# Kernel optimization log

Hardware: AMD Instinct MI355X
Metric: run time of the kernel (lower is better)

Reference implementation:

```python
import jax, jax.numpy as jnp
import numpy as np


def _rotate_half(x):
    x1, x2 = jnp.split(x, 2, axis=-1)
    return jnp.concatenate([-x2, x1], axis=-1)


def _rope_tables(seq_len, head_dim, base=10000.0):
    inv_freq = 1.0 / (base ** (jnp.arange(0, head_dim, 2, dtype=jnp.float32) / head_dim))
    t = jnp.arange(seq_len, dtype=jnp.float32)
    freqs = jnp.outer(t, inv_freq)  # [S, head_dim/2]
    # torch .repeat(...,2) tiles along last dim -> concat
    cos = jnp.concatenate([jnp.cos(freqs), jnp.cos(freqs)], axis=-1)  # [S, head_dim]
    sin = jnp.concatenate([jnp.sin(freqs), jnp.sin(freqs)], axis=-1)
    return cos[None, None], sin[None, None]  # [1,1,S,head_dim]


def setup_inputs() -> dict:
    key = jax.random.key(0)
    ks = jax.random.split(key, 5)
    B, S, D = 2, 2048, 2048
    sd = 1.0 / np.sqrt(D)
    return {
        "x": jax.random.normal(ks[0], (B, S, D), dtype=jnp.float32),
        "Wq": jax.random.normal(ks[1], (D, D), dtype=jnp.float32) * sd,
        "Wk": jax.random.normal(ks[2], (D, D), dtype=jnp.float32) * sd,
        "Wv": jax.random.normal(ks[3], (D, D), dtype=jnp.float32) * sd,
        "Wo": jax.random.normal(ks[4], (D, D), dtype=jnp.float32) * sd,
        "n_heads": 16,
    }


def reference(x, Wq, Wk, Wv, Wo, n_heads):
    B, S, D = x.shape
    hd = D // n_heads
    # projections (torch Linear: x @ W.T)
    def proj(W):
        return (x @ W.T).reshape(B, S, n_heads, hd).transpose(0, 2, 1, 3)  # [B,H,S,hd]
    q, k, v = proj(Wq), proj(Wk), proj(Wv)
    cos, sin = _rope_tables(S, hd)
    q = q * cos + _rotate_half(q) * sin
    k = k * cos + _rotate_half(k) * sin
    scale = 1.0 / np.sqrt(hd)
    scores = jnp.einsum('bhsd,bhtd->bhst', q, k) * scale  # [B,H,S,S]
    causal = jnp.triu(jnp.ones((S, S), dtype=bool), k=1)
    scores = jnp.where(causal[None, None], -jnp.inf, scores)
    attn = jax.nn.softmax(scores, axis=-1)
    out = jnp.einsum('bhst,bhtd->bhsd', attn, v)
    out = out.transpose(0, 2, 1, 3).reshape(B, S, D)
    return out @ Wo.T
```

## Files before the change

kernel.cpp:

```cpp
#include <hip/hip_runtime.h>
#include <hip/hip_bf16.h>
#include <math.h>

typedef __attribute__((ext_vector_type(8))) short bf16x8;
typedef __attribute__((ext_vector_type(4))) float f32x4;

#define GLB_CAST(p) ((const __attribute__((address_space(1))) void*)(p))
#define LDS_CAST(p) ((__attribute__((address_space(3))) void*)(p))

__global__ void cvt_f32_bf16(const float* __restrict__ s, __hip_bfloat16* __restrict__ d, int n) {
    int i = (blockIdx.x * 256 + threadIdx.x) * 8;
    if (i >= n) return;
    float4 a = *(const float4*)(s + i);
    float4 b = *(const float4*)(s + i + 4);
    float t[8] = {a.x, a.y, a.z, a.w, b.x, b.y, b.z, b.w};
    union { unsigned short u[8]; uint4 v; } o;
#pragma unroll
    for (int j = 0; j < 8; ++j) {
        __hip_bfloat16 h = __float2bfloat16(t[j]);
        o.u[j] = *(unsigned short*)&h;
    }
    *(uint4*)(d + i) = o.v;
}

template <int EPI>
__global__ __launch_bounds__(256, 2)
void gemm_bt(const __hip_bfloat16* __restrict__ A,
             const __hip_bfloat16* __restrict__ Bt,
             void* __restrict__ Cout)
{
    const int K = 2048;
    __shared__ __hip_bfloat16 As[128 * 32];
    __shared__ __hip_bfloat16 Bs[128 * 32];
    const int tid = threadIdx.x;
    const int w = tid >> 6, l = tid & 63;
    const int m0 = blockIdx.x * 128, n0 = blockIdx.y * 128;
    const int wr = w >> 1, wc = w & 1;
    const int lr = l & 15, kh = l >> 4;

    f32x4 acc[4][4] = {};

    for (int kt = 0; kt < 64; ++kt) {
        const int kb = kt * 32;
#pragma unroll
        for (int i = 0; i < 2; ++i) {
            const int s = i * 256 + tid;
            const int r = s >> 2, ks = (s & 3) * 8;
            __builtin_amdgcn_global_load_lds(GLB_CAST(A + (size_t)(m0 + r) * K + kb + ks),
                                             LDS_CAST(As + (size_t)(i * 256 + w * 64) * 8),
                                             16, 0, 0);
            __builtin_amdgcn_global_load_lds(GLB_CAST(Bt + (size_t)(n0 + r) * K + kb + ks),
                                             LDS_CAST(Bs + (size_t)(i * 256 + w * 64) * 8),
                                             16, 0, 0);
        }
        __syncthreads();
        bf16x8 af[4], bfr[4];
#pragma unroll
        for (int m = 0; m < 4; ++m)
            af[m] = *(const bf16x8*)(As + (wr * 64 + m * 16 + lr) * 32 + kh * 8);
#pragma unroll
        for (int n = 0; n < 4; ++n)
            bfr[n] = *(const bf16x8*)(Bs + (wc * 64 + n * 16 + lr) * 32 + kh * 8);
#pragma unroll
        for (int m = 0; m < 4; ++m)
#pragma unroll
            for (int n = 0; n < 4; ++n)
                acc[m][n] = __builtin_amdgcn_mfma_f32_16x16x32_bf16(af[m], bfr[n], acc[m][n], 0, 0, 0);
        __syncthreads();
    }

#pragma unroll
    for (int m = 0; m < 4; ++m) {
        const int r0 = m0 + wr * 64 + m * 16 + kh * 4;
#pragma unroll
        for (int n = 0; n < 4; ++n) {
            const int c = n0 + wc * 64 + n * 16 + lr;
#pragma unroll
            for (int j = 0; j < 4; ++j) {
                const int r = r0 + j;
                const float v = acc[m][n][j];
                if (EPI == 0) {
                    const int b = r >> 11, sy = r & 2047, h = c >> 7, dd = c & 127;
                    ((__hip_bfloat16*)Cout)[((size_t)(b * 16 + h) * 2048 + sy) * 128 + dd] =
                        __float2bfloat16(v);
                } else if (EPI == 2) {
                    const int b = r >> 11, sy = r & 2047, h = c >> 7, dd = c & 127;
                    ((__hip_bfloat16*)Cout)[((size_t)(b * 16 + h) * 128 + dd) * 2048 + sy] =
                        __float2bfloat16(v);
                } else {
                    ((float*)Cout)[(size_t)r * 2048 + c] = v;
                }
            }
        }
    }
}

__global__ void rope_qk(__hip_bfloat16* __restrict__ Q, __hip_bfloat16* __restrict__ Kk) {
    const int row = blockIdx.x * 4 + (threadIdx.x >> 6);
    const int j = threadIdx.x & 63;
    const int s = row & 2047;
    const float inv = expf((float)j * (-0.14391156831212787f));
    float sn, c;
    sincosf((float)s * inv, &sn, &c);
    const size_t base = (size_t)row * 128;
    float q1 = __bfloat162float(Q[base + j]);
    float q2 = __bfloat162float(Q[base + 64 + j]);
    Q[base + j]      = __float2bfloat16(q1 * c - q2 * sn);
    Q[base + 64 + j] = __float2bfloat16(q2 * c + q1 * sn);
    float k1 = __bfloat162float(Kk[base + j]);
    float k2 = __bfloat162float(Kk[base + 64 + j]);
    Kk[base + j]      = __float2bfloat16(k1 * c - k2 * sn);
    Kk[base + 64 + j] = __float2bfloat16(k2 * c + k1 * sn);
}

__global__ __launch_bounds__(256, 4)
void flash_part(const __hip_bfloat16* __restrict__ Q,
                const __hip_bfloat16* __restrict__ K,
                const __hip_bfloat16* __restrict__ Vt,
                __hip_bfloat16* __restrict__ AO,
                __hip_bfloat16* __restrict__ OP,
                float* __restrict__ ML)
{
    const int bh = blockIdx.x;
    const int u  = blockIdx.y;
    const int tid = threadIdx.x, w = tid >> 6, l = tid & 63;
    const int lr = l & 15, hi = l >> 4;

    int G, part, P;
    if (u < 32)      { G = 24 + (u >> 2);            part = u & 3;       P = 4; }
    else if (u < 56) { int v = u - 32; G = 16 + v/3; part = v % 3;       P = 3; }
    else if (u < 72) { int v = u - 56; G = 8 + (v>>1); part = v & 1;     P = 2; }
    else             { G = u - 72;                   part = 0;           P = 1; }
    const int nt = 2 * G + 2;
    const int t0 = (part * nt) / P, t1 = ((part + 1) * nt) / P;
    const bool split = (P > 1);
    const int qb = G * 64 + w * 16;

    const __hip_bfloat16* Qb = Q  + (size_t)bh * 2048 * 128;
    const __hip_bfloat16* Kb = K  + (size_t)bh * 2048 * 128;
    const __hip_bfloat16* Vb = Vt + (size_t)bh * 128 * 2048;

    __shared__ __align__(16) __hip_bfloat16 Ks[2][32 * 128];
    __shared__ __align__(16) __hip_bfloat16 Vs[2][128 * 32];
    __shared__ __align__(16) __hip_bfloat16 Pl[4][16 * 40];
    __hip_bfloat16* Pw = &Pl[w][0];

    bf16x8 qf[4];
#pragma unroll
    for (int kk = 0; kk < 4; ++kk)
        qf[kk] = *(const bf16x8*)(Qb + (size_t)(qb + lr) * 128 + kk * 32 + hi * 8);

    int rK[2], cK[2], rV[2], cV[2];
#pragma unroll
    for (int i = 0; i < 2; ++i) {
        const int ci = i * 4 + w;
        rK[i] = ci * 4 + (l >> 4);
        cK[i] = ((l & 15) ^ (rK[i] & 7)) * 8;
        rV[i] = ci * 16 + (l >> 2);
        cV[i] = ((l & 3) ^ (rV[i] & 3)) * 8;
    }
    const int rsw7 = lr & 7, vsw3 = lr & 3;

#define STAGE(buf, t)                                                                        \
    {                                                                                        \
        const int kv0_ = (t) * 32;                                                           \
        _Pragma("unroll")                                                                    \
        for (int i = 0; i < 2; ++i) {                                                        \
            __builtin_amdgcn_global_load_lds(                                                \
                GLB_CAST(Kb + (size_t)(kv0_ + rK[i]) * 128 + cK[i]),                         \
                LDS_CAST(&Ks[buf][(i * 4 + w) * 512]), 16, 0, 0);                            \
            __builtin_amdgcn_global_load_lds(                                                \
                GLB_CAST(Vb + (size_t)rV[i] * 2048 + kv0_ + cV[i]),                          \
                LDS_CAST(&Vs[buf][(i * 4 + w) * 512]), 16, 0, 0);                            \
        }                                                                                    \
    }

    f32x4 o[8] = {};
    float mrow[4] = {-1e30f, -1e30f, -1e30f, -1e30f};
    float lrow[4] = {0.f, 0.f, 0.f, 0.f};
    const float scale = 0.08838834764831845f;

    int cur = 0;
    STAGE(0, t0);
    __syncthreads();

    for (int t = t0; t < t1; ++t) {
        if (t + 1 < t1) STAGE(cur ^ 1, t + 1);
        const __hip_bfloat16* Kc = &Ks[cur][0];
        const __hip_bfloat16* Vc = &Vs[cur][0];
        const int kv0 = t * 32;

        f32x4 sf[2] = {};
#pragma unroll
        for (int f = 0; f < 2; ++f)
#pragma unroll
            for (int kk = 0; kk < 4; ++kk) {
                const bf16x8 kf = *(const bf16x8*)(Kc + (f * 16 + lr) * 128 +
                                                   ((kk * 4 + hi) ^ rsw7) * 8);
                sf[f] = __builtin_amdgcn_mfma_f32_16x16x32_bf16(qf[kk], kf, sf[f], 0, 0, 0);
            }

        float alpha[4];
#pragma unroll
        for (int j = 0; j < 4; ++j) {
            const int q = qb + hi * 4 + j;
            float s0v = sf[0][j] * scale; if (kv0 + lr > q)      s0v = -1e30f;
            float s1v = sf[1][j] * scale; if (kv0 + 16 + lr > q) s1v = -1e30f;
            float mx = fmaxf(s0v, s1v);
#pragma unroll
            for (int dd = 1; dd < 16; dd <<= 1)
                mx = fmaxf(mx, __shfl_xor(mx, dd));
            const float mnew = fmaxf(mrow[j], mx);
            alpha[j] = __expf(mrow[j] - mnew);
            mrow[j] = mnew;
            const float p0 = __expf(s0v - mnew);
            const float p1 = __expf(s1v - mnew);
            float rs = p0 + p1;
#pragma unroll
            for (int dd = 1; dd < 16; dd <<= 1)
                rs += __shfl_xor(rs, dd);
            lrow[j] = lrow[j] * alpha[j] + rs;
            Pw[(hi * 4 + j) * 40 + lr]      = __float2bfloat16(p0);
            Pw[(hi * 4 + j) * 40 + 16 + lr] = __float2bfloat16(p1);
        }
#pragma unroll
        for (int dn = 0; dn < 8; ++dn)
#pragma unroll
            for (int j = 0; j < 4; ++j) o[dn][j] *= alpha[j];

        const bf16x8 pf = *(const bf16x8*)(Pw + lr * 40 + hi * 8);
#pragma unroll
        for (int dn = 0; dn < 8; ++dn) {
            const bf16x8 vf = *(const bf16x8*)(Vc + (dn * 16 + lr) * 32 + (hi ^ vsw3) * 8);
            o[dn] = __builtin_amdgcn_mfma_f32_16x16x32_bf16(pf, vf, o[dn], 0, 0, 0);
        }
        __syncthreads();
        cur ^= 1;
    }
#undef STAGE

    if (!split) {
#pragma unroll
        for (int j = 0; j < 4; ++j) {
            const float inv = 1.0f / lrow[j];
            const int q = qb + hi * 4 + j;
            const size_t rb = ((size_t)(bh >> 4) * 2048 + q) * 2048 + (size_t)(bh & 15) * 128;
#pragma unroll
            for (int dn = 0; dn < 8; ++dn)
                AO[rb + dn * 16 + lr] = __float2bfloat16(o[dn][j] * inv);
        }
    } else {
        const int base = (G < 16) ? (G - 8) * 2 : ((G < 24) ? 16 + (G - 16) * 3
                                                            : 40 + (G - 24) * 4);
        const int pidx = bh * 72 + base + part;
#pragma unroll
        for (int j = 0; j < 4; ++j) {
            const int row = w * 16 + hi * 4 + j;
#pragma unroll
            for (int dn = 0; dn < 8; ++dn)
                OP[((size_t)pidx * 64 + row) * 128 + dn * 16 + lr] = __float2bfloat16(o[dn][j]);
            if (lr == 0) {
                ML[((size_t)pidx * 64 + row) * 2]     = mrow[j];
                ML[((size_t)pidx * 64 + row) * 2 + 1] = lrow[j];
            }
        }
    }
}

__global__ void flash_merge(const __hip_bfloat16* __restrict__ OP,
                            const float* __restrict__ ML,
                            __hip_bfloat16* __restrict__ AO)
{
    const int gi = blockIdx.x % 24, bh = blockIdx.x / 24;
    const int G = 8 + gi;
    const int P = (G < 16) ? 2 : ((G < 24) ? 3 : 4);
    const int base = (G < 16) ? (G - 8) * 2 : ((G < 24) ? 16 + (G - 16) * 3
                                                        : 40 + (G - 24) * 4);
    const int pidx0 = bh * 72 + base;
    const int t = threadIdx.x, r = t >> 2, c0 = (t & 3) * 32;

    float m[4], lv[4];
    float M = -1e30f;
#pragma unroll
    for (int p = 0; p < 4; ++p) if (p < P) {
        m[p]  = ML[((size_t)(pidx0 + p) * 64 + r) * 2];
        lv[p] = ML[((size_t)(pidx0 + p) * 64 + r) * 2 + 1];
        M = fmaxf(M, m[p]);
    }
    float wgt[4];
    float den = 0.f;
#pragma unroll
    for (int p = 0; p < 4; ++p) if (p < P) {
        wgt[p] = __expf(m[p] - M);
        den += lv[p] * wgt[p];
    }
    const float inv = 1.0f / den;

    const int q = G * 64 + r;
    __hip_bfloat16* out = AO + ((size_t)(bh >> 4) * 2048 + q) * 2048 + (size_t)(bh & 15) * 128 + c0;

#pragma unroll
    for (int ch = 0; ch < 4; ++ch) {
        float acc[8] = {0.f, 0.f, 0.f, 0.f, 0.f, 0.f, 0.f, 0.f};
#pragma unroll
        for (int p = 0; p < 4; ++p) if (p < P) {
            const bf16x8 v = *(const bf16x8*)(OP + ((size_t)(pidx0 + p) * 64 + r) * 128 + c0 + ch * 8);
#pragma unroll
            for (int i = 0; i < 8; ++i) {
                __hip_bfloat16 hv;
                *(short*)&hv = v[i];
                acc[i] += __bfloat162float(hv) * wgt[p];
            }
        }
        union { unsigned short us[8]; bf16x8 v; } rr;
#pragma unroll
        for (int i = 0; i < 8; ++i) {
            __hip_bfloat16 hv = __float2bfloat16(acc[i] * inv);
            rr.us[i] = *(unsigned short*)&hv;
        }
        *(bf16x8*)(out + ch * 8) = rr.v;
    }
}

extern "C" void kernel_launch(void* const* d_in, const int* in_sizes, int n_in,
                              void* d_out, int out_size, void* d_ws, size_t ws_size,
                              hipStream_t stream) {
    (void)in_sizes; (void)n_in; (void)out_size; (void)ws_size;
    const float* x  = (const float*)d_in[0];
    const float* Wq = (const float*)d_in[1];
    const float* Wk = (const float*)d_in[2];
    const float* Wv = (const float*)d_in[3];
    const float* Wo = (const float*)d_in[4];

    char* p = (char*)d_ws;
    auto carve = [&](size_t bytes) -> char* {
        char* r = p;
        p += (bytes + 255) & ~(size_t)255;
        return r;
    };
    __hip_bfloat16* xb  = (__hip_bfloat16*)carve(4096ull * 2048 * 2);
    __hip_bfloat16* Wqb = (__hip_bfloat16*)carve(2048ull * 2048 * 2);
    __hip_bfloat16* Wkb = (__hip_bfloat16*)carve(2048ull * 2048 * 2);
    __hip_bfloat16* Wvb = (__hip_bfloat16*)carve(2048ull * 2048 * 2);
    __hip_bfloat16* Wob = (__hip_bfloat16*)carve(2048ull * 2048 * 2);
    __hip_bfloat16* Qb  = (__hip_bfloat16*)carve(32ull * 2048 * 128 * 2);
    __hip_bfloat16* Kb  = (__hip_bfloat16*)carve(32ull * 2048 * 128 * 2);
    __hip_bfloat16* Vtb = (__hip_bfloat16*)carve(32ull * 128 * 2048 * 2);
    __hip_bfloat16* OPb = (__hip_bfloat16*)carve(32ull * 72 * 64 * 128 * 2);
    float*          MLb = (float*)carve(32ull * 72 * 64 * 2 * 4);

    cvt_f32_bf16<<<4096, 256, 0, stream>>>(x,  xb,  4096 * 2048);
    cvt_f32_bf16<<<2048, 256, 0, stream>>>(Wq, Wqb, 2048 * 2048);
    cvt_f32_bf16<<<2048, 256, 0, stream>>>(Wk, Wkb, 2048 * 2048);
    cvt_f32_bf16<<<2048, 256, 0, stream>>>(Wv, Wvb, 2048 * 2048);
    cvt_f32_bf16<<<2048, 256, 0, stream>>>(Wo, Wob, 2048 * 2048);

    dim3 gg(32, 16);
    gemm_bt<0><<<gg, 256, 0, stream>>>(xb, Wqb, Qb);
    gemm_bt<0><<<gg, 256, 0, stream>>>(xb, Wkb, Kb);
    gemm_bt<2><<<gg, 256, 0, stream>>>(xb, Wvb, Vtb);

    rope_qk<<<16384, 256, 0, stream>>>(Qb, Kb);

    flash_part<<<dim3(32, 80), 256, 0, stream>>>(Qb, Kb, Vtb, xb , OPb, MLb);
    flash_merge<<<768, 256, 0, stream>>>(OPb, MLb, xb );

    gemm_bt<1><<<gg, 256, 0, stream>>>(xb, Wob, (float*)d_out);
}
```

Baseline: 356.2 us.

## Compute transposed S tiles in flash attention and pass P through register shuffles

The QK^T MFMA operands are swapped so each lane owns one query row's scores across the KV block. This turns the per-row max and sum reductions into two cross-lane shuffles and lets the P fragment be built by register shuffles instead of an LDS round-trip. It also adds a lazy rescale that skips the O rescaling while the running max has grown by no more than 8, and switches the RoPE kernel to fast __expf/__sincosf intrinsics. The cost is extra shuffles to rebuild the P fragment and broadcast alpha, and some lost precision in the RoPE angles.

```diff
diff --git a/kernel.cpp b/kernel.cpp
--- a/kernel.cpp
+++ b/kernel.cpp
@@ -7,6 +7,11 @@
 
 #define GLB_CAST(p) ((const __attribute__((address_space(1))) void*)(p))
 #define LDS_CAST(p) ((__attribute__((address_space(3))) void*)(p))
+
+static __device__ __forceinline__ unsigned short bf16_bits(float x) {
+    __hip_bfloat16 h = __float2bfloat16(x);
+    return *(unsigned short*)&h;
+}
 
 __global__ void cvt_f32_bf16(const float* __restrict__ s, __hip_bfloat16* __restrict__ d, int n) {
     int i = (blockIdx.x * 256 + threadIdx.x) * 8;
@@ -16,10 +21,7 @@
     float t[8] = {a.x, a.y, a.z, a.w, b.x, b.y, b.z, b.w};
     union { unsigned short u[8]; uint4 v; } o;
 #pragma unroll
-    for (int j = 0; j < 8; ++j) {
-        __hip_bfloat16 h = __float2bfloat16(t[j]);
-        o.u[j] = *(unsigned short*)&h;
-    }
+    for (int j = 0; j < 8; ++j) o.u[j] = bf16_bits(t[j]);
     *(uint4*)(d + i) = o.v;
 }
 
@@ -99,9 +101,9 @@
     const int row = blockIdx.x * 4 + (threadIdx.x >> 6);
     const int j = threadIdx.x & 63;
     const int s = row & 2047;
-    const float inv = expf((float)j * (-0.14391156831212787f));
+    const float inv = __expf((float)j * (-0.14391156831212787f));
     float sn, c;
-    sincosf((float)s * inv, &sn, &c);
+    __sincosf((float)s * inv, &sn, &c);
     const size_t base = (size_t)row * 128;
     float q1 = __bfloat162float(Q[base + j]);
     float q2 = __bfloat162float(Q[base + 64 + j]);
@@ -135,6 +137,7 @@
     const int t0 = (part * nt) / P, t1 = ((part + 1) * nt) / P;
     const bool split = (P > 1);
     const int qb = G * 64 + w * 16;
+    const int q_own = qb + lr;
 
     const __hip_bfloat16* Qb = Q  + (size_t)bh * 2048 * 128;
     const __hip_bfloat16* Kb = K  + (size_t)bh * 2048 * 128;
@@ -142,8 +145,6 @@
 
     __shared__ __align__(16) __hip_bfloat16 Ks[2][32 * 128];
     __shared__ __align__(16) __hip_bfloat16 Vs[2][128 * 32];
-    __shared__ __align__(16) __hip_bfloat16 Pl[4][16 * 40];
-    __hip_bfloat16* Pw = &Pl[w][0];
 
     bf16x8 qf[4];
 #pragma unroll
@@ -160,6 +161,9 @@
         cV[i] = ((l & 3) ^ (rV[i] & 3)) * 8;
     }
     const int rsw7 = lr & 7, vsw3 = lr & 3;
+    const int sA = lr + ((hi & 1) << 5);
+    const int sB = sA + 16;
+    const bool plo = (hi < 2);
 
 #define STAGE(buf, t)                                                                        \
     {                                                                                        \
@@ -176,8 +180,7 @@
     }
 
     f32x4 o[8] = {};
-    float mrow[4] = {-1e30f, -1e30f, -1e30f, -1e30f};
-    float lrow[4] = {0.f, 0.f, 0.f, 0.f};
+    float mrow = -1e30f, lrow = 0.f;
     const float scale = 0.08838834764831845f;
 
     int cur = 0;
@@ -190,64 +193,91 @@
         const __hip_bfloat16* Vc = &Vs[cur][0];
         const int kv0 = t * 32;
 
-        f32x4 sf[2] = {};
+        f32x4 sT[2] = {};
 #pragma unroll
         for (int f = 0; f < 2; ++f)
 #pragma unroll
             for (int kk = 0; kk < 4; ++kk) {
                 const bf16x8 kf = *(const bf16x8*)(Kc + (f * 16 + lr) * 128 +
                                                    ((kk * 4 + hi) ^ rsw7) * 8);
-                sf[f] = __builtin_amdgcn_mfma_f32_16x16x32_bf16(qf[kk], kf, sf[f], 0, 0, 0);
+                sT[f] = __builtin_amdgcn_mfma_f32_16x16x32_bf16(kf, qf[kk], sT[f], 0, 0, 0);
             }
 
-        float alpha[4];
+        float val[8];
+        float pmax = -1e30f;
+#pragma unroll
+        for (int f = 0; f < 2; ++f)
+#pragma unroll
+            for (int j = 0; j < 4; ++j) {
+                const int kv = kv0 + f * 16 + hi * 4 + j;
+                float v = sT[f][j] * scale;
+                v = (kv > q_own) ? -1e30f : v;
+                val[f * 4 + j] = v;
+                pmax = fmaxf(pmax, v);
+            }
+        pmax = fmaxf(pmax, __shfl_xor(pmax, 16));
+        pmax = fmaxf(pmax, __shfl_xor(pmax, 32));
+
+        if (!__all(pmax <= mrow + 8.f)) {
+            const float mnew = fmaxf(mrow, pmax);
+            const float alpha = __expf(mrow - mnew);
+            mrow = mnew;
+            lrow *= alpha;
+            float aj[4];
+#pragma unroll
+            for (int j = 0; j < 4; ++j)
+                aj[j] = __shfl(alpha, (l & 48) | (hi * 4 + j), 64);
+#pragma unroll
+            for (int dn = 0; dn < 8; ++dn)
+#pragma unroll
+                for (int j = 0; j < 4; ++j) o[dn][j] *= aj[j];
+        }
+
+        float p[8];
+        float rs = 0.f;
+#pragma unroll
+        for (int i = 0; i < 8; ++i) { p[i] = __expf(val[i] - mrow); rs += p[i]; }
+        rs += __shfl_xor(rs, 16);
+        rs += __shfl_xor(rs, 32);
+        lrow += rs;
+
+        unsigned wds[4];
+#pragma unroll
+        for (int i = 0; i < 4; ++i)
+            wds[i] = (unsigned)bf16_bits(p[i * 2]) | ((unsigned)bf16_bits(p[i * 2 + 1]) << 16);
+
+        const unsigned a0 = __shfl((int)wds[0], sA, 64), a1 = __shfl((int)wds[1], sA, 64);
+        const unsigned a2 = __shfl((int)wds[2], sA, 64), a3 = __shfl((int)wds[3], sA, 64);
+        const unsigned b0 = __shfl((int)wds[0], sB, 64), b1 = __shfl((int)wds[1], sB, 64);
+        const unsigned b2 = __shfl((int)wds[2], sB, 64), b3 = __shfl((int)wds[3], sB, 64);
+        union { unsigned u[4]; bf16x8 v; } pf;
+        pf.u[0] = plo ? a0 : a2;
+        pf.u[1] = plo ? a1 : a3;
+        pf.u[2] = plo ? b0 : b2;
+        pf.u[3] = plo ? b1 : b3;
+
+#pragma unroll
+        for (int dn = 0; dn < 8; ++dn) {
+            const bf16x8 vf = *(const bf16x8*)(Vc + (dn * 16 + lr) * 32 + (hi ^ vsw3) * 8);
+            o[dn] = __builtin_amdgcn_mfma_f32_16x16x32_bf16(pf.v, vf, o[dn], 0, 0, 0);
+        }
+        __syncthreads();
+        cur ^= 1;
+    }
+#undef STAGE
+
+    if (!split) {
+        float linv[4];
+#pragma unroll
+        for (int j = 0; j < 4; ++j)
+            linv[j] = 1.0f / __shfl(lrow, (l & 48) | (hi * 4 + j), 64);
 #pragma unroll
         for (int j = 0; j < 4; ++j) {
             const int q = qb + hi * 4 + j;
-            float s0v = sf[0][j] * scale; if (kv0 + lr > q)      s0v = -1e30f;
-            float s1v = sf[1][j] * scale; if (kv0 + 16 + lr > q) s1v = -1e30f;
-            float mx = fmaxf(s0v, s1v);
-#pragma unroll
-            for (int dd = 1; dd < 16; dd <<= 1)
-                mx = fmaxf(mx, __shfl_xor(mx, dd));
-            const float mnew = fmaxf(mrow[j], mx);
-            alpha[j] = __expf(mrow[j] - mnew);
-            mrow[j] = mnew;
-            const float p0 = __expf(s0v - mnew);
-            const float p1 = __expf(s1v - mnew);
-            float rs = p0 + p1;
-#pragma unroll
-            for (int dd = 1; dd < 16; dd <<= 1)
-                rs += __shfl_xor(rs, dd);
-            lrow[j] = lrow[j] * alpha[j] + rs;
-            Pw[(hi * 4 + j) * 40 + lr]      = __float2bfloat16(p0);
-            Pw[(hi * 4 + j) * 40 + 16 + lr] = __float2bfloat16(p1);
-        }
-#pragma unroll
-        for (int dn = 0; dn < 8; ++dn)
-#pragma unroll
-            for (int j = 0; j < 4; ++j) o[dn][j] *= alpha[j];
-
-        const bf16x8 pf = *(const bf16x8*)(Pw + lr * 40 + hi * 8);
-#pragma unroll
-        for (int dn = 0; dn < 8; ++dn) {
-            const bf16x8 vf = *(const bf16x8*)(Vc + (dn * 16 + lr) * 32 + (hi ^ vsw3) * 8);
-            o[dn] = __builtin_amdgcn_mfma_f32_16x16x32_bf16(pf, vf, o[dn], 0, 0, 0);
-        }
-        __syncthreads();
-        cur ^= 1;
-    }
-#undef STAGE
-
-    if (!split) {
-#pragma unroll
-        for (int j = 0; j < 4; ++j) {
-            const float inv = 1.0f / lrow[j];
-            const int q = qb + hi * 4 + j;
             const size_t rb = ((size_t)(bh >> 4) * 2048 + q) * 2048 + (size_t)(bh & 15) * 128;
 #pragma unroll
             for (int dn = 0; dn < 8; ++dn)
-                AO[rb + dn * 16 + lr] = __float2bfloat16(o[dn][j] * inv);
+                AO[rb + dn * 16 + lr] = __float2bfloat16(o[dn][j] * linv[j]);
         }
     } else {
         const int base = (G < 16) ? (G - 8) * 2 : ((G < 24) ? 16 + (G - 16) * 3
@@ -259,10 +289,10 @@
 #pragma unroll
             for (int dn = 0; dn < 8; ++dn)
                 OP[((size_t)pidx * 64 + row) * 128 + dn * 16 + lr] = __float2bfloat16(o[dn][j]);
-            if (lr == 0) {
-                ML[((size_t)pidx * 64 + row) * 2]     = mrow[j];
-                ML[((size_t)pidx * 64 + row) * 2 + 1] = lrow[j];
-            }
+        }
+        if (l < 16) {
+            ML[((size_t)pidx * 64 + w * 16 + l) * 2]     = mrow;
+            ML[((size_t)pidx * 64 + w * 16 + l) * 2 + 1] = lrow;
         }
     }
 }
@@ -314,10 +344,7 @@
         }
         union { unsigned short us[8]; bf16x8 v; } rr;
 #pragma unroll
-        for (int i = 0; i < 8; ++i) {
-            __hip_bfloat16 hv = __float2bfloat16(acc[i] * inv);
-            rr.us[i] = *(unsigned short*)&hv;
-        }
+        for (int i = 0; i < 8; ++i) rr.us[i] = bf16_bits(acc[i] * inv);
         *(bf16x8*)(out + ch * 8) = rr.v;
     }
 }
```

Measured after the change: 322.5 us. 1.1x faster.
